# Kernel tuning notes

Measured on AMD Instinct MI355X. Metric: run time of the kernel, lower is better.

## Reference

```python
import jax, jax.numpy as jnp
import numpy as np

H = 4  # hidden_size
I = 2  # input_size
T = 50  # seq_len
B = 262144  # batch
OUT = 1


def _lstm_layer(x, Wih, Whh, bih, bhh):
    # x: [T, B, in]; PyTorch gate order i, f, g, o in rows of Wih/Whh.
    b = bih + bhh
    h0 = jnp.zeros((x.shape[1], Whh.shape[1]), x.dtype)
    c0 = jnp.zeros_like(h0)

    def step(carry, xt):
        h, c = carry
        gates = xt @ Wih.T + h @ Whh.T + b  # [B, 4H]
        i, f, g, o = jnp.split(gates, 4, axis=-1)
        c = jax.nn.sigmoid(f) * c + jax.nn.sigmoid(i) * jnp.tanh(g)
        h = jax.nn.sigmoid(o) * jnp.tanh(c)
        return (h, c), h

    (_, _), ys = jax.lax.scan(step, (h0, c0), x)
    return ys  # [T, B, H]


def setup_inputs() -> dict:
    key = jax.random.key(0)
    ks = jax.random.split(key, 11)
    s = 1.0 / np.sqrt(H)  # PyTorch LSTM/Linear init scale
    u = lambda k, shp: jax.random.uniform(k, shp, jnp.float32, -s, s)
    x = jax.random.normal(ks[0], (B, T, I), jnp.float32)
    return {
        "x": x,
        "Wih0": u(ks[1], (4 * H, I)),
        "Whh0": u(ks[2], (4 * H, H)),
        "bih0": u(ks[3], (4 * H,)),
        "bhh0": u(ks[4], (4 * H,)),
        "Wih1": u(ks[5], (4 * H, H)),
        "Whh1": u(ks[6], (4 * H, H)),
        "bih1": u(ks[7], (4 * H,)),
        "bhh1": u(ks[8], (4 * H,)),
        "Wout": jax.random.uniform(ks[9], (OUT, H * T), jnp.float32, -1.0 / np.sqrt(H * T), 1.0 / np.sqrt(H * T)),
        "bout": jax.random.uniform(ks[10], (OUT,), jnp.float32, -1.0 / np.sqrt(H * T), 1.0 / np.sqrt(H * T)),
    }


def reference(x, Wih0, Whh0, bih0, bhh0, Wih1, Whh1, bih1, bhh1, Wout, bout):
    xt = jnp.transpose(x, (1, 0, 2))  # [T, B, I]
    y = _lstm_layer(xt, Wih0, Whh0, bih0, bhh0)  # [T, B, H]
    y = _lstm_layer(y, Wih1, Whh1, bih1, bhh1)   # [T, B, H]
    y = jnp.transpose(y, (1, 0, 2)).reshape(x.shape[0], -1)  # [B, T*H]
    return jax.nn.sigmoid(y @ Wout.T + bout)  # [B, 1]
```

## Files before the change

### kernel.cpp

```cpp
#include <hip/hip_runtime.h>

#define T_LEN 50

typedef __fp16 fp16x8 __attribute__((ext_vector_type(8)));
typedef float f32x16 __attribute__((ext_vector_type(16)));
typedef unsigned int uint4v __attribute__((ext_vector_type(4)));

__device__ __forceinline__ float EXP2(float x){ return __builtin_amdgcn_exp2f(x); }
__device__ __forceinline__ float RCP(float x){ return __builtin_amdgcn_rcpf(x); }
__device__ __forceinline__ unsigned PKU(float a, float b){
    return __builtin_bit_cast(unsigned, __builtin_amdgcn_cvt_pkrtz(a, b));
}

__device__ __forceinline__ void act(float gi, float gf, float gg, float go,
                                    float& c, float& h){
    const float S2 = -2.8853900817779268f;
    const float p = EXP2(gi);
    const float r = EXP2(gf);
    const float q = EXP2(gg);
    const float s = EXP2(go);
    const float A  = 1.0f + r;
    const float BC = (1.0f + p) * (1.0f + q);
    const float num = fmaf(c, BC, (1.0f - q) * A);
    c = num * RCP(A * BC);
    const float u = EXP2(fminf(c * S2, 96.0f));
    h = (1.0f - u) * RCP((1.0f + s) * (1.0f + u));
}

__global__ __launch_bounds__(256, 6) void lstm_mfma32(
    const float* __restrict__ x,
    const float* __restrict__ Wih0, const float* __restrict__ Whh0,
    const float* __restrict__ bih0, const float* __restrict__ bhh0,
    const float* __restrict__ Wih1, const float* __restrict__ Whh1,
    const float* __restrict__ bih1, const float* __restrict__ bhh1,
    const float* __restrict__ Wout, const float* __restrict__ bout,
    float* __restrict__ out, int B)
{
    __shared__ float2 wout_s[T_LEN*2];
    __shared__ unsigned xstage[4*32*T_LEN];
    const int tid = threadIdx.x;
    if (tid < T_LEN*2){
        const int t = tid >> 1, hh = tid & 1;
        wout_s[tid] = make_float2(Wout[t*4+hh], Wout[t*4+hh+2]);
    }
    __syncthreads();

    const int lane = tid & 63;
    const int e = lane & 31;
    const int h = lane >> 5;
    const int wslot = tid >> 6;
    const int wave = (blockIdx.x*256 + tid) >> 6;
    const int E0 = wave * 32;
    if (E0 >= B) return;

    unsigned* xr = xstage + wslot * (32*T_LEN);

    const float S1 = -1.4426950408889634f;
    const float S2 = -2.8853900817779268f;

    const int qA = e >> 2, tA = e & 3;
    const float sA = (tA == 2) ? S2 : S1;
    uint4v au;
#pragma unroll
    for (int p = 0; p < 4; ++p){
        float vv[2];
#pragma unroll
        for (int z = 0; z < 2; ++z){
            const int k = 8*h + 2*p + z;
            float v = 0.f;
            if (qA < 4){
                const int r = tA*4 + qA;
                if (k < 2)      v = Wih0[r*2 + k];
                else if (k < 6) v = Whh0[r*4 + (k-2)];
            } else {
                const int r = tA*4 + (qA-4);
                if (k >= 2 && k < 6)       v = Wih1[r*4 + (k-2)];
                else if (k >= 6 && k < 10) v = Whh1[r*4 + (k-6)];
            }
            vv[z] = v * sA;
        }
        au[p] = PKU(vv[0], vv[1]);
    }
    const fp16x8 Afrag = __builtin_bit_cast(fp16x8, au);

    f32x16 biasC;
#pragma unroll
    for (int r = 0; r < 16; ++r){
        const int m = (r&3) + 8*(r>>2) + 4*h;
        const int q = m >> 2, tg = m & 3;
        const float st = (tg == 2) ? S2 : S1;
        if (q < 4){ const int rr = tg*4 + q;      biasC[r] = (bih0[rr]+bhh0[rr])*st; }
        else      { const int rr = tg*4 + (q-4);  biasC[r] = (bih1[rr]+bhh1[rr])*st; }
    }

    const float* xg = x + (size_t)E0 * (T_LEN*2);

#pragma unroll
    for (int k = 0; k < 25; ++k){
        const int i = 64*k + lane;
        const int e_ = i / T_LEN, t_ = i % T_LEN;
        const float2 v = *reinterpret_cast<const float2*>(xg + e_*100 + t_*2);
        xr[e_*T_LEN + t_] = PKU(v.x, v.y);
    }

    float c0l=0.f, c0h=0.f, c1l=0.f, c1h=0.f, acc=0.f;
    unsigned pk_h0_01=0u, pk_h0_23=0u, pk_h1_01=0u, pk_h1_23=0u;

    auto mainstep = [&](int t, unsigned ux){
        uint4v bu;
        bu[0] = h ? pk_h1_23 : ux;
        bu[1] = pk_h0_01;
        bu[2] = pk_h0_23;
        bu[3] = pk_h1_01;
        const f32x16 d = __builtin_amdgcn_mfma_f32_32x32x16_f16(
            Afrag, __builtin_bit_cast(fp16x8, bu), biasC, 0, 0, 0);
        float h0l,h0h,h1l,h1h;
        act(d[0], d[1], d[2], d[3],  c0l, h0l);
        act(d[4], d[5], d[6], d[7],  c0h, h0h);
        act(d[8], d[9], d[10],d[11], c1l, h1l);
        act(d[12],d[13],d[14],d[15], c1h, h1h);
        const float2 wo = wout_s[(t-1)*2 + h];
        acc = fmaf(h1l, wo.x, fmaf(h1h, wo.y, acc));
        const float r0l = __shfl_xor(h0l,32,64), r0h = __shfl_xor(h0h,32,64);
        const float r1l = __shfl_xor(h1l,32,64), r1h = __shfl_xor(h1h,32,64);
        pk_h0_01 = PKU(h0l, r0l);
        pk_h0_23 = PKU(h0h, r0h);
        pk_h1_01 = PKU(h1l, r1l);
        pk_h1_23 = PKU(r1h, h1h);
    };

    {
        const unsigned ux = xr[e*T_LEN + 0];
        uint4v bu; bu[0] = h ? 0u : ux; bu[1]=0u; bu[2]=0u; bu[3]=0u;
        const f32x16 d = __builtin_amdgcn_mfma_f32_32x32x16_f16(
            Afrag, __builtin_bit_cast(fp16x8, bu), biasC, 0, 0, 0);
        float h0l, h0h;
        act(d[0],d[1],d[2],d[3], c0l, h0l);
        act(d[4],d[5],d[6],d[7], c0h, h0h);
        const float r0l = __shfl_xor(h0l, 32, 64);
        const float r0h = __shfl_xor(h0h, 32, 64);
        pk_h0_01 = PKU(h0l, r0l);
        pk_h0_23 = PKU(h0h, r0h);
    }

    for (int t = 1; t < T_LEN; ++t)
        mainstep(t, xr[e*T_LEN + t]);

    {
        uint4v bu;
        bu[0] = h ? pk_h1_23 : 0u;
        bu[1] = pk_h0_01; bu[2] = pk_h0_23; bu[3] = pk_h1_01;
        const f32x16 d = __builtin_amdgcn_mfma_f32_32x32x16_f16(
            Afrag, __builtin_bit_cast(fp16x8, bu), biasC, 0, 0, 0);
        float h1l, h1h;
        act(d[8], d[9], d[10],d[11], c1l, h1l);
        act(d[12],d[13],d[14],d[15], c1h, h1h);
        const float2 wo = wout_s[49*2 + h];
        acc = fmaf(h1l, wo.x, fmaf(h1h, wo.y, acc));
    }

    acc += __shfl_xor(acc, 32, 64);
    if (h == 0){
        const float z = acc + bout[0];
        out[E0 + e] = RCP(1.0f + EXP2(z * S1));
    }
}

extern "C" void kernel_launch(void* const* d_in, const int* in_sizes, int n_in,
                              void* d_out, int out_size, void* d_ws, size_t ws_size,
                              hipStream_t stream)
{
    const float* x    = (const float*)d_in[0];
    const float* Wih0 = (const float*)d_in[1];
    const float* Whh0 = (const float*)d_in[2];
    const float* bih0 = (const float*)d_in[3];
    const float* bhh0 = (const float*)d_in[4];
    const float* Wih1 = (const float*)d_in[5];
    const float* Whh1 = (const float*)d_in[6];
    const float* bih1 = (const float*)d_in[7];
    const float* bhh1 = (const float*)d_in[8];
    const float* Wout = (const float*)d_in[9];
    const float* bout = (const float*)d_in[10];
    float* out = (float*)d_out;

    const int B = in_sizes[0] / (T_LEN*2);
    const int waves = (B + 31) / 32;
    const int blocks = (waves + 3) / 4;
    lstm_mfma32<<<blocks, 256, 0, stream>>>(x, Wih0, Whh0, bih0, bhh0,
                                            Wih1, Whh1, bih1, bhh1,
                                            Wout, bout, out, B);
}
```

Measured before the change: 92.40 us.

## Interleave two independent batch tiles per wave to hide MFMA and transcendental latency

Each wave now processes 64 batch elements as two independent 32-element recurrences, interleaving their MFMA and activation chains within each timestep. The goal is instruction-level parallelism that hides the serial latency of the MFMA, exp2 and shuffle chain in each recurrence step. Block size drops to 128 threads with a lower occupancy hint, and the fp16 packing switches from round-toward-zero to round-to-nearest conversion. The cost is higher register pressure and fewer resident waves, since twice the state is kept per wave.

```diff
diff --git a/kernel.cpp b/kernel.cpp
--- a/kernel.cpp
+++ b/kernel.cpp
@@ -8,8 +8,10 @@
 
 __device__ __forceinline__ float EXP2(float x){ return __builtin_amdgcn_exp2f(x); }
 __device__ __forceinline__ float RCP(float x){ return __builtin_amdgcn_rcpf(x); }
-__device__ __forceinline__ unsigned PKU(float a, float b){
-    return __builtin_bit_cast(unsigned, __builtin_amdgcn_cvt_pkrtz(a, b));
+__device__ __forceinline__ unsigned PKN(float a, float b){
+    const unsigned short ua = __builtin_bit_cast(unsigned short, (_Float16)a);
+    const unsigned short ub = __builtin_bit_cast(unsigned short, (_Float16)b);
+    return (unsigned)ua | ((unsigned)ub << 16);
 }
 
 __device__ __forceinline__ void act(float gi, float gf, float gg, float go,
@@ -27,7 +29,12 @@
     h = (1.0f - u) * RCP((1.0f + s) * (1.0f + u));
 }
 
-__global__ __launch_bounds__(256, 6) void lstm_mfma32(
+struct TS {
+    float c0l, c0h, c1l, c1h, acc;
+    unsigned p0, p1, p2, p3;
+};
+
+__global__ __launch_bounds__(128, 3) void lstm_mfma32(
     const float* __restrict__ x,
     const float* __restrict__ Wih0, const float* __restrict__ Whh0,
     const float* __restrict__ bih0, const float* __restrict__ bhh0,
@@ -37,7 +44,7 @@
     float* __restrict__ out, int B)
 {
     __shared__ float2 wout_s[T_LEN*2];
-    __shared__ unsigned xstage[4*32*T_LEN];
+    __shared__ unsigned xstage[2*64*T_LEN];
     const int tid = threadIdx.x;
     if (tid < T_LEN*2){
         const int t = tid >> 1, hh = tid & 1;
@@ -49,11 +56,11 @@
     const int e = lane & 31;
     const int h = lane >> 5;
     const int wslot = tid >> 6;
-    const int wave = (blockIdx.x*256 + tid) >> 6;
-    const int E0 = wave * 32;
+    const int wave = (blockIdx.x*128 + tid) >> 6;
+    const int E0 = wave * 64;
     if (E0 >= B) return;
 
-    unsigned* xr = xstage + wslot * (32*T_LEN);
+    unsigned* xr = xstage + wslot * (64*T_LEN);
 
     const float S1 = -1.4426950408889634f;
     const float S2 = -2.8853900817779268f;
@@ -79,7 +86,7 @@
             }
             vv[z] = v * sA;
         }
-        au[p] = PKU(vv[0], vv[1]);
+        au[p] = PKN(vv[0], vv[1]);
     }
     const fp16x8 Afrag = __builtin_bit_cast(fp16x8, au);
 
@@ -95,74 +102,88 @@
 
     const float* xg = x + (size_t)E0 * (T_LEN*2);
 
-#pragma unroll
-    for (int k = 0; k < 25; ++k){
+#pragma unroll 10
+    for (int k = 0; k < 50; ++k){
         const int i = 64*k + lane;
         const int e_ = i / T_LEN, t_ = i % T_LEN;
         const float2 v = *reinterpret_cast<const float2*>(xg + e_*100 + t_*2);
-        xr[e_*T_LEN + t_] = PKU(v.x, v.y);
-    }
-
-    float c0l=0.f, c0h=0.f, c1l=0.f, c1h=0.f, acc=0.f;
-    unsigned pk_h0_01=0u, pk_h0_23=0u, pk_h1_01=0u, pk_h1_23=0u;
-
-    auto mainstep = [&](int t, unsigned ux){
+        xr[e_*T_LEN + t_] = PKN(v.x, v.y);
+    }
+
+    TS sA_, sB_;
+    sA_.c0l=0.f; sA_.c0h=0.f; sA_.c1l=0.f; sA_.c1h=0.f; sA_.acc=0.f;
+    sA_.p0=0u; sA_.p1=0u; sA_.p2=0u; sA_.p3=0u;
+    sB_ = sA_;
+
+    const unsigned* xrA = xr + e*T_LEN;
+    const unsigned* xrB = xr + (32+e)*T_LEN;
+
+    auto mstep = [&](TS& st, unsigned ux, float2 wo){
         uint4v bu;
-        bu[0] = h ? pk_h1_23 : ux;
-        bu[1] = pk_h0_01;
-        bu[2] = pk_h0_23;
-        bu[3] = pk_h1_01;
+        bu[0] = h ? st.p3 : ux;
+        bu[1] = st.p0;
+        bu[2] = st.p1;
+        bu[3] = st.p2;
         const f32x16 d = __builtin_amdgcn_mfma_f32_32x32x16_f16(
             Afrag, __builtin_bit_cast(fp16x8, bu), biasC, 0, 0, 0);
         float h0l,h0h,h1l,h1h;
-        act(d[0], d[1], d[2], d[3],  c0l, h0l);
-        act(d[4], d[5], d[6], d[7],  c0h, h0h);
-        act(d[8], d[9], d[10],d[11], c1l, h1l);
-        act(d[12],d[13],d[14],d[15], c1h, h1h);
-        const float2 wo = wout_s[(t-1)*2 + h];
-        acc = fmaf(h1l, wo.x, fmaf(h1h, wo.y, acc));
+        act(d[0], d[1], d[2], d[3],   st.c0l, h0l);
+        act(d[4], d[5], d[6], d[7],   st.c0h, h0h);
+        act(d[8], d[9], d[10],d[11],  st.c1l, h1l);
+        act(d[12],d[13],d[14],d[15],  st.c1h, h1h);
+        st.acc = fmaf(h1l, wo.x, fmaf(h1h, wo.y, st.acc));
         const float r0l = __shfl_xor(h0l,32,64), r0h = __shfl_xor(h0h,32,64);
         const float r1l = __shfl_xor(h1l,32,64), r1h = __shfl_xor(h1h,32,64);
-        pk_h0_01 = PKU(h0l, r0l);
-        pk_h0_23 = PKU(h0h, r0h);
-        pk_h1_01 = PKU(h1l, r1l);
-        pk_h1_23 = PKU(r1h, h1h);
+        st.p0 = PKN(h0l, r0l);
+        st.p1 = PKN(h0h, r0h);
+        st.p2 = PKN(h1l, r1l);
+        st.p3 = PKN(r1h, h1h);
     };
 
-    {
-        const unsigned ux = xr[e*T_LEN + 0];
+    auto prol = [&](TS& st, unsigned ux){
         uint4v bu; bu[0] = h ? 0u : ux; bu[1]=0u; bu[2]=0u; bu[3]=0u;
         const f32x16 d = __builtin_amdgcn_mfma_f32_32x32x16_f16(
             Afrag, __builtin_bit_cast(fp16x8, bu), biasC, 0, 0, 0);
         float h0l, h0h;
-        act(d[0],d[1],d[2],d[3], c0l, h0l);
-        act(d[4],d[5],d[6],d[7], c0h, h0h);
+        act(d[0],d[1],d[2],d[3], st.c0l, h0l);
+        act(d[4],d[5],d[6],d[7], st.c0h, h0h);
         const float r0l = __shfl_xor(h0l, 32, 64);
         const float r0h = __shfl_xor(h0h, 32, 64);
-        pk_h0_01 = PKU(h0l, r0l);
-        pk_h0_23 = PKU(h0h, r0h);
-    }
-
-    for (int t = 1; t < T_LEN; ++t)
-        mainstep(t, xr[e*T_LEN + t]);
-
-    {
+        st.p0 = PKN(h0l, r0l);
+        st.p1 = PKN(h0h, r0h);
+    };
+
+    prol(sA_, xrA[0]);
+    prol(sB_, xrB[0]);
+
+    for (int t = 1; t < T_LEN; ++t){
+        const unsigned xa = xrA[t];
+        const unsigned xb = xrB[t];
+        const float2 wo = wout_s[(t-1)*2 + h];
+        mstep(sA_, xa, wo);
+        mstep(sB_, xb, wo);
+    }
+
+    auto epil = [&](TS& st, float2 wo) -> float {
         uint4v bu;
-        bu[0] = h ? pk_h1_23 : 0u;
-        bu[1] = pk_h0_01; bu[2] = pk_h0_23; bu[3] = pk_h1_01;
+        bu[0] = h ? st.p3 : 0u;
+        bu[1] = st.p0; bu[2] = st.p1; bu[3] = st.p2;
         const f32x16 d = __builtin_amdgcn_mfma_f32_32x32x16_f16(
             Afrag, __builtin_bit_cast(fp16x8, bu), biasC, 0, 0, 0);
         float h1l, h1h;
-        act(d[8], d[9], d[10],d[11], c1l, h1l);
-        act(d[12],d[13],d[14],d[15], c1h, h1h);
-        const float2 wo = wout_s[49*2 + h];
-        acc = fmaf(h1l, wo.x, fmaf(h1h, wo.y, acc));
-    }
-
-    acc += __shfl_xor(acc, 32, 64);
+        act(d[8], d[9], d[10],d[11],  st.c1l, h1l);
+        act(d[12],d[13],d[14],d[15],  st.c1h, h1h);
+        return fmaf(h1l, wo.x, fmaf(h1h, wo.y, st.acc));
+    };
+    const float2 wo49 = wout_s[49*2 + h];
+    float aA = epil(sA_, wo49);
+    float aB = epil(sB_, wo49);
+
+    aA += __shfl_xor(aA, 32, 64);
+    aB += __shfl_xor(aB, 32, 64);
     if (h == 0){
-        const float z = acc + bout[0];
-        out[E0 + e] = RCP(1.0f + EXP2(z * S1));
+        out[E0 + e]      = RCP(1.0f + EXP2((aA + bout[0]) * S1));
+        out[E0 + 32 + e] = RCP(1.0f + EXP2((aB + bout[0]) * S1));
     }
 }
 
@@ -184,9 +205,9 @@
     float* out = (float*)d_out;
 
     const int B = in_sizes[0] / (T_LEN*2);
-    const int waves = (B + 31) / 32;
-    const int blocks = (waves + 3) / 4;
-    lstm_mfma32<<<blocks, 256, 0, stream>>>(x, Wih0, Whh0, bih0, bhh0,
+    const int waves = (B + 63) / 64;
+    const int blocks = (waves + 1) / 2;
+    lstm_mfma32<<<blocks, 128, 0, stream>>>(x, Wih0, Whh0, bih0, bhh0,
                                             Wih1, Whh1, bih1, bhh1,
                                             Wout, bout, out, B);
 }
```

After: 123.5 us. 33.6% more time.
